# Kernel tuning notes

Measured on AMD Instinct MI355X. Metric: run time of the kernel, lower is better.

## Reference

```python
import jax, jax.numpy as jnp
import numpy as np

K = 10
ALPHA = 0.1
N_NODES = 100000
N_EDGES = 3200000
IN_CH, HID_CH, OUT_CH = 500, 64, 16


def setup_inputs() -> dict:
    key = jax.random.key(0)
    k1, k2, k3, k4, k5, k6 = jax.random.split(key, 6)
    x = jax.random.normal(k1, (N_NODES, IN_CH), dtype=jnp.float32)
    edge_index = jax.random.randint(k2, (2, N_EDGES), 0, N_NODES, dtype=jnp.int64)
    # Linear params (Kaiming-uniform-ish scale)
    s1 = 1.0 / np.sqrt(IN_CH)
    s2 = 1.0 / np.sqrt(HID_CH)
    W1 = jax.random.uniform(k3, (IN_CH, HID_CH), dtype=jnp.float32, minval=-s1, maxval=s1)
    b1 = jax.random.uniform(k4, (HID_CH,), dtype=jnp.float32, minval=-s1, maxval=s1)
    W2 = jax.random.uniform(k5, (HID_CH, OUT_CH), dtype=jnp.float32, minval=-s2, maxval=s2)
    b2 = jax.random.uniform(k6, (OUT_CH,), dtype=jnp.float32, minval=-s2, maxval=s2)
    return {"x": x, "edge_index": edge_index, "W1": W1, "b1": b1, "W2": W2, "b2": b2}


def reference(x, edge_index, W1, b1, W2, b2):
    N = x.shape[0]
    # MLP (eval mode: dropout is identity)
    h = jnp.maximum(x @ W1 + b1, 0.0)
    h = h @ W2 + b2  # [N, out_channels]

    # GCN normalization with self-loops (PyG gcn_norm defaults)
    loops = jnp.arange(N, dtype=edge_index.dtype)
    row = jnp.concatenate([edge_index[0], loops])  # source
    col = jnp.concatenate([edge_index[1], loops])  # target
    ones = jnp.ones(row.shape[0], dtype=h.dtype)
    deg = jax.ops.segment_sum(ones, col, num_segments=N)
    dinv = jnp.where(deg > 0, jax.lax.rsqrt(deg), 0.0)
    norm = dinv[row] * dinv[col]  # [E+N]

    # K-step APPNP propagation: h_{k+1} = (1-alpha) * A_hat h_k + alpha * h_0
    h0 = h

    def step(_, hk):
        agg = jax.ops.segment_sum(norm[:, None] * hk[row], col, num_segments=N)
        return (1.0 - ALPHA) * agg + ALPHA * h0

    return jax.lax.fori_loop(0, K, step, h)
```

## Files before the change

kernel.cpp:

```cpp
#include <hip/hip_runtime.h>

#define IN_CH 500
#define KSTEPS 10

typedef unsigned int u32;
typedef unsigned short u16;
typedef short bf16x8 __attribute__((ext_vector_type(8)));
typedef float f32x4 __attribute__((ext_vector_type(4)));

__device__ __forceinline__ float bf2f(u16 u) {
    union { u32 i; float f; } v; v.i = ((u32)u) << 16; return v.f;
}
__device__ __forceinline__ u16 f2bf(float f) {
    union { float f; u32 i; } v; v.f = f;
    u32 x = v.i;
    return (u16)((x + 0x7FFFu + ((x >> 16) & 1u)) >> 16);
}
__device__ __forceinline__ u32 f_as_u(float f) {
    union { float f; u32 i; } v; v.f = f; return v.i;
}
__device__ __forceinline__ float u_as_f(u32 i) {
    union { u32 i; float f; } v; v.i = i; return v.f;
}

__global__ void detect_kernel(const u16* __restrict__ w1raw,
                              const int* __restrict__ ei,
                              u32* __restrict__ flags) {
    int t = threadIdx.x;
    float m = fabsf(bf2f(w1raw[t]));
    m = fmaxf(m, fabsf(bf2f(w1raw[64 + t])));
    m = fmaxf(m, fabsf(bf2f(w1raw[128 + t])));
    for (int off = 32; off; off >>= 1) m = fmaxf(m, __shfl_down(m, off));
    u32 o = (u32)ei[2 * t + 1];
    o |= (u32)ei[2 * t + 129];
    for (int off = 32; off; off >>= 1) o |= __shfl_down(o, off);
    if (t == 0) {
        flags[0] = (m > 10.0f) ? 1u : 0u;
        flags[1] = (o == 0u) ? 1u : 0u;
    }
}

__global__ void w1t_kernel(const void* __restrict__ W1v,
                           u16* __restrict__ hi, u16* __restrict__ lo,
                           const u32* __restrict__ flags) {
    int i = blockIdx.x * 256 + threadIdx.x;
    if (i >= 64 * 512) return;
    int h = i >> 9;
    int k = i & 511;
    u16 vh = 0, vl = 0;
    if (k < IN_CH) {
        if (flags[0]) {
            float v = ((const float*)W1v)[(size_t)k * 64 + h];
            u32 bits = f_as_u(v);
            vh = (u16)(bits >> 16);
            float d = v - u_as_f(bits & 0xFFFF0000u);
            vl = (u16)(f_as_u(d) >> 16);
        } else {
            vh = ((const u16*)W1v)[(size_t)k * 64 + h];
        }
    }
    hi[(size_t)h * 512 + k] = vh;
    lo[(size_t)h * 512 + k] = vl;
}

__global__ __launch_bounds__(512) void mlp_mfma_f32(
    const float* __restrict__ xf, const u16* __restrict__ w1hig,
    const u16* __restrict__ w1log, const float* __restrict__ b1f,
    const float* __restrict__ W2f, const float* __restrict__ b2f,
    const float* __restrict__ dinv, float* __restrict__ h0,
    float* __restrict__ gout, const u32* __restrict__ flags, int N)
{
    if (flags[0] == 0u) return;

    __shared__ __align__(16) u16 w1hi[64 * 520];
    __shared__ __align__(16) u16 w1lo[64 * 520];
    __shared__ float w2s[64][16];
    __shared__ float b1s[64];
    __shared__ float b2s[16];
    float* hh = (float*)w1hi;

    const int t = threadIdx.x;
    const int w = t >> 6;
    const int l = t & 63;
    const int ln = l & 15;
    const int g = l >> 4;
    const int nodeBase = blockIdx.x * 128;

    for (int i = t; i < 1024; i += 512) w2s[i >> 4][i & 15] = W2f[i];
    if (t < 64) b1s[t] = b1f[t];
    if (t < 16) b2s[t] = b2f[t];

#pragma unroll
    for (int i = 0; i < 8; ++i) {
        int c = t + i * 512;
        int row = c >> 6, c8 = c & 63;
        *(bf16x8*)&w1hi[row * 520 + c8 * 8] =
            *(const bf16x8*)(w1hig + (size_t)row * 512 + c8 * 8);
        *(bf16x8*)&w1lo[row * 520 + c8 * 8] =
            *(const bf16x8*)(w1log + (size_t)row * 512 + c8 * 8);
    }
    __syncthreads();

    const int node = nodeBase + w * 16 + ln;
    const bool nv = (node < N);
    const float* xrow = xf + (size_t)node * IN_CH;

    f32x4 acc0 = {0.f, 0.f, 0.f, 0.f};
    f32x4 acc1 = {0.f, 0.f, 0.f, 0.f};
    f32x4 acc2 = {0.f, 0.f, 0.f, 0.f};
    f32x4 acc3 = {0.f, 0.f, 0.f, 0.f};

#pragma unroll
    for (int ki = 0; ki < 16; ++ki) {
        const int kb = ki * 32 + g * 8;
        float xv[8];
#pragma unroll
        for (int e = 0; e < 8; ++e) xv[e] = 0.f;
        if (nv) {
            if (kb + 8 <= IN_CH) {
                float4 v0 = *(const float4*)(xrow + kb);
                float4 v1 = *(const float4*)(xrow + kb + 4);
                xv[0] = v0.x; xv[1] = v0.y; xv[2] = v0.z; xv[3] = v0.w;
                xv[4] = v1.x; xv[5] = v1.y; xv[6] = v1.z; xv[7] = v1.w;
            } else if (kb < IN_CH) {
                float4 v0 = *(const float4*)(xrow + kb);
                xv[0] = v0.x; xv[1] = v0.y; xv[2] = v0.z; xv[3] = v0.w;
            }
        }
        bf16x8 bh, bl;
#pragma unroll
        for (int e = 0; e < 8; ++e) {
            u32 bits = f_as_u(xv[e]);
            bh[e] = (short)(bits >> 16);
            float d = xv[e] - u_as_f(bits & 0xFFFF0000u);
            bl[e] = (short)(f_as_u(d) >> 16);
        }
        const u16* ph = &w1hi[ln * 520 + kb];
        const u16* pl = &w1lo[ln * 520 + kb];
        bf16x8 ah0 = *(const bf16x8*)(ph);
        bf16x8 ah1 = *(const bf16x8*)(ph + 16 * 520);
        bf16x8 ah2 = *(const bf16x8*)(ph + 32 * 520);
        bf16x8 ah3 = *(const bf16x8*)(ph + 48 * 520);
        bf16x8 al0 = *(const bf16x8*)(pl);
        bf16x8 al1 = *(const bf16x8*)(pl + 16 * 520);
        bf16x8 al2 = *(const bf16x8*)(pl + 32 * 520);
        bf16x8 al3 = *(const bf16x8*)(pl + 48 * 520);
        acc0 = __builtin_amdgcn_mfma_f32_16x16x32_bf16(ah0, bh, acc0, 0, 0, 0);
        acc1 = __builtin_amdgcn_mfma_f32_16x16x32_bf16(ah1, bh, acc1, 0, 0, 0);
        acc2 = __builtin_amdgcn_mfma_f32_16x16x32_bf16(ah2, bh, acc2, 0, 0, 0);
        acc3 = __builtin_amdgcn_mfma_f32_16x16x32_bf16(ah3, bh, acc3, 0, 0, 0);
        acc0 = __builtin_amdgcn_mfma_f32_16x16x32_bf16(al0, bh, acc0, 0, 0, 0);
        acc1 = __builtin_amdgcn_mfma_f32_16x16x32_bf16(al1, bh, acc1, 0, 0, 0);
        acc2 = __builtin_amdgcn_mfma_f32_16x16x32_bf16(al2, bh, acc2, 0, 0, 0);
        acc3 = __builtin_amdgcn_mfma_f32_16x16x32_bf16(al3, bh, acc3, 0, 0, 0);
        acc0 = __builtin_amdgcn_mfma_f32_16x16x32_bf16(ah0, bl, acc0, 0, 0, 0);
        acc1 = __builtin_amdgcn_mfma_f32_16x16x32_bf16(ah1, bl, acc1, 0, 0, 0);
        acc2 = __builtin_amdgcn_mfma_f32_16x16x32_bf16(ah2, bl, acc2, 0, 0, 0);
        acc3 = __builtin_amdgcn_mfma_f32_16x16x32_bf16(ah3, bl, acc3, 0, 0, 0);
    }
    __syncthreads();

    const int nl = w * 16 + ln;
    const int rb = g * 4;
#pragma unroll
    for (int r = 0; r < 4; ++r) {
        float v0 = acc0[r] + b1s[rb + r];
        float v1 = acc1[r] + b1s[16 + rb + r];
        float v2 = acc2[r] + b1s[32 + rb + r];
        float v3 = acc3[r] + b1s[48 + rb + r];
        hh[(rb + r) * 130 + nl]      = v0 > 0.f ? v0 : 0.f;
        hh[(16 + rb + r) * 130 + nl] = v1 > 0.f ? v1 : 0.f;
        hh[(32 + rb + r) * 130 + nl] = v2 > 0.f ? v2 : 0.f;
        hh[(48 + rb + r) * 130 + nl] = v3 > 0.f ? v3 : 0.f;
    }
    __syncthreads();

    {
        int n = t >> 2;
        int o4 = (t & 3) * 4;
        float o0 = b2s[o4], o1 = b2s[o4 + 1], o2 = b2s[o4 + 2], o3 = b2s[o4 + 3];
#pragma unroll
        for (int j = 0; j < 64; ++j) {
            float hv = hh[j * 130 + n];
            o0 += hv * w2s[j][o4];     o1 += hv * w2s[j][o4 + 1];
            o2 += hv * w2s[j][o4 + 2]; o3 += hv * w2s[j][o4 + 3];
        }
        int gn = nodeBase + n;
        if (gn < N) {
            float4 o = {o0, o1, o2, o3};
            *(float4*)(h0 + (size_t)gn * 16 + o4) = o;
            float dn = dinv[gn];
            float4 gg = {o0 * dn, o1 * dn, o2 * dn, o3 * dn};
            *(float4*)(gout + (size_t)gn * 16 + o4) = gg;
        }
    }
}

__global__ __launch_bounds__(256) void mlp_mfma_kernel(
    const u16* __restrict__ xh, const u16* __restrict__ w1tg,
    const void* __restrict__ b1v, const void* __restrict__ W2v,
    const void* __restrict__ b2v, const float* __restrict__ dinv,
    float* __restrict__ h0, float* __restrict__ gout,
    const u32* __restrict__ flags, int N)
{
    if (flags[0] != 0u) return;

    __shared__ __align__(16) u16 w1s[64 * 520];
    __shared__ float w2s[64][16];
    __shared__ float b1s[64];
    __shared__ float b2s[16];
    float* hh = (float*)w1s;

    const u16* b1h = (const u16*)b1v;
    const u16* W2h = (const u16*)W2v;
    const u16* b2h = (const u16*)b2v;

    const int t = threadIdx.x;
    const int w = t >> 6;
    const int l = t & 63;
    const int ln = l & 15;
    const int g = l >> 4;
    const int nodeBase = blockIdx.x * 64;

    for (int i = t; i < 1024; i += 256) w2s[i >> 4][i & 15] = bf2f(W2h[i]);
    if (t < 64) b1s[t] = bf2f(b1h[t]);
    if (t < 16) b2s[t] = bf2f(b2h[t]);

#pragma unroll
    for (int i = 0; i < 16; ++i) {
        int idx = t + i * 256;
        int row = idx >> 6, c8 = idx & 63;
        *(bf16x8*)&w1s[row * 520 + c8 * 8] =
            *(const bf16x8*)(w1tg + (size_t)row * 512 + c8 * 8);
    }
    __syncthreads();

    const int node = nodeBase + w * 16 + ln;
    const bool nv = (node < N);
    const u16* xrow = xh + (size_t)node * IN_CH;

    f32x4 acc0 = {0.f, 0.f, 0.f, 0.f};
    f32x4 acc1 = {0.f, 0.f, 0.f, 0.f};
    f32x4 acc2 = {0.f, 0.f, 0.f, 0.f};
    f32x4 acc3 = {0.f, 0.f, 0.f, 0.f};

#pragma unroll
    for (int ki = 0; ki < 15; ++ki) {
        const int kb = ki * 32 + g * 8;
        bf16x8 b = {0, 0, 0, 0, 0, 0, 0, 0};
        if (nv) b = *(const bf16x8*)(xrow + kb);
        const u16* wp = &w1s[ln * 520 + kb];
        bf16x8 a0 = *(const bf16x8*)(wp);
        bf16x8 a1 = *(const bf16x8*)(wp + 16 * 520);
        bf16x8 a2 = *(const bf16x8*)(wp + 32 * 520);
        bf16x8 a3 = *(const bf16x8*)(wp + 48 * 520);
        acc0 = __builtin_amdgcn_mfma_f32_16x16x32_bf16(a0, b, acc0, 0, 0, 0);
        acc1 = __builtin_amdgcn_mfma_f32_16x16x32_bf16(a1, b, acc1, 0, 0, 0);
        acc2 = __builtin_amdgcn_mfma_f32_16x16x32_bf16(a2, b, acc2, 0, 0, 0);
        acc3 = __builtin_amdgcn_mfma_f32_16x16x32_bf16(a3, b, acc3, 0, 0, 0);
    }
    {
        const int kb = 480 + g * 8;
        bf16x8 b = {0, 0, 0, 0, 0, 0, 0, 0};
        if (nv) {
            if (g < 2) {
                b = *(const bf16x8*)(xrow + kb);
            } else if (g == 2) {
                ushort4 v4 = *(const ushort4*)(xrow + 496);
                b[0] = (short)v4.x; b[1] = (short)v4.y;
                b[2] = (short)v4.z; b[3] = (short)v4.w;
            }
        }
        const u16* wp = &w1s[ln * 520 + kb];
        bf16x8 a0 = *(const bf16x8*)(wp);
        bf16x8 a1 = *(const bf16x8*)(wp + 16 * 520);
        bf16x8 a2 = *(const bf16x8*)(wp + 32 * 520);
        bf16x8 a3 = *(const bf16x8*)(wp + 48 * 520);
        acc0 = __builtin_amdgcn_mfma_f32_16x16x32_bf16(a0, b, acc0, 0, 0, 0);
        acc1 = __builtin_amdgcn_mfma_f32_16x16x32_bf16(a1, b, acc1, 0, 0, 0);
        acc2 = __builtin_amdgcn_mfma_f32_16x16x32_bf16(a2, b, acc2, 0, 0, 0);
        acc3 = __builtin_amdgcn_mfma_f32_16x16x32_bf16(a3, b, acc3, 0, 0, 0);
    }
    __syncthreads();

    const int nl = w * 16 + ln;
    const int rb = g * 4;
#pragma unroll
    for (int r = 0; r < 4; ++r) {
        float v0 = acc0[r] + b1s[rb + r];
        float v1 = acc1[r] + b1s[16 + rb + r];
        float v2 = acc2[r] + b1s[32 + rb + r];
        float v3 = acc3[r] + b1s[48 + rb + r];
        hh[(rb + r) * 65 + nl]      = v0 > 0.f ? v0 : 0.f;
        hh[(16 + rb + r) * 65 + nl] = v1 > 0.f ? v1 : 0.f;
        hh[(32 + rb + r) * 65 + nl] = v2 > 0.f ? v2 : 0.f;
        hh[(48 + rb + r) * 65 + nl] = v3 > 0.f ? v3 : 0.f;
    }
    __syncthreads();

    {
        int n = t >> 2;
        int o4 = (t & 3) * 4;
        float o0 = b2s[o4], o1 = b2s[o4 + 1], o2 = b2s[o4 + 2], o3 = b2s[o4 + 3];
#pragma unroll
        for (int j = 0; j < 64; ++j) {
            float hv = hh[j * 65 + n];
            o0 += hv * w2s[j][o4];     o1 += hv * w2s[j][o4 + 1];
            o2 += hv * w2s[j][o4 + 2]; o3 += hv * w2s[j][o4 + 3];
        }
        int gn = nodeBase + n;
        if (gn < N) {
            float4 o = {o0, o1, o2, o3};
            *(float4*)(h0 + (size_t)gn * 16 + o4) = o;
            float dn = dinv[gn];
            float4 gg = {o0 * dn, o1 * dn, o2 * dn, o3 * dn};
            *(float4*)(gout + (size_t)gn * 16 + o4) = gg;
        }
    }
}

__global__ void zero_u32(u32* __restrict__ p, int n) {
    int i = blockIdx.x * 256 + threadIdx.x;
    if (i < n) p[i] = 0u;
}

__device__ __forceinline__ int ei_src(const int* ei, int E, int e, int i64) {
    return i64 ? ei[2 * e] : ei[e];
}
__device__ __forceinline__ int ei_dst(const int* ei, int E, int e, int i64) {
    return i64 ? ei[2 * (E + e)] : ei[E + e];
}

__global__ void deg_kernel(const int* __restrict__ ei, int E, u32* __restrict__ cnt,
                           const u32* __restrict__ flags) {
    int e = blockIdx.x * 256 + threadIdx.x;
    int i64 = (int)flags[1];
    if (e < E) atomicAdd(&cnt[ei_dst(ei, E, e, i64)], 1u);
}

__global__ void dinv_kernel(const u32* __restrict__ cnt, float* __restrict__ dinv, int N) {
    int i = blockIdx.x * 256 + threadIdx.x;
    if (i < N) {
        float d = (float)(cnt[i] + 1u);
        dinv[i] = rsqrtf(d);
    }
}

__global__ __launch_bounds__(256) void scan1(const u32* __restrict__ cnt,
                                             u32* __restrict__ part, int N) {
    __shared__ u32 s[256];
    int i = blockIdx.x * 256 + threadIdx.x;
    s[threadIdx.x] = (i < N) ? cnt[i] : 0u;
    __syncthreads();
    for (int off = 128; off > 0; off >>= 1) {
        if (threadIdx.x < off) s[threadIdx.x] += s[threadIdx.x + off];
        __syncthreads();
    }
    if (threadIdx.x == 0) part[blockIdx.x] = s[0];
}

__global__ __launch_bounds__(512) void scan2(u32* __restrict__ part,
                                             u32* __restrict__ rowptr, int NB, int N) {
    __shared__ u32 s[512];
    int t = threadIdx.x;
    u32 v = (t < NB) ? part[t] : 0u;
    s[t] = v;
    __syncthreads();
    for (int off = 1; off < 512; off <<= 1) {
        u32 xv = (t >= off) ? s[t - off] : 0u;
        __syncthreads();
        s[t] += xv;
        __syncthreads();
    }
    if (t < NB) part[t] = s[t] - v;
    if (t == 511) rowptr[N] = s[511];
}

__global__ __launch_bounds__(256) void scan3(const u32* __restrict__ cnt,
                                             const u32* __restrict__ part,
                                             u32* __restrict__ rowptr, int N) {
    __shared__ u32 s[256];
    int t = threadIdx.x;
    int i = blockIdx.x * 256 + t;
    u32 v = (i < N) ? cnt[i] : 0u;
    s[t] = v;
    __syncthreads();
    for (int off = 1; off < 256; off <<= 1) {
        u32 xv = (t >= off) ? s[t - off] : 0u;
        __syncthreads();
        s[t] += xv;
        __syncthreads();
    }
    if (i < N) rowptr[i] = part[blockIdx.x] + s[t] - v;
}

#define GSZ_SHIFT 9
#define GSZ 512
#define MAXBUCK 1024
__global__ void init_bf(const u32* __restrict__ rowptr, u32* __restrict__ bf,
                        int N, int nbuck) {
    int t = blockIdx.x * 256 + threadIdx.x;
    if (t < nbuck) {
        int lo = t << GSZ_SHIFT; if (lo > N) lo = N;
        bf[t] = rowptr[lo];
    }
}

#define CHUNK 4096
__global__ __launch_bounds__(256) void bucketA(
    const int* __restrict__ ei, int E, int shiftN, int nbuck,
    u32* __restrict__ tmp, u32* __restrict__ bf, const u32* __restrict__ flags)
{
    __shared__ u32 wbuf[CHUNK];
    __shared__ u16 bbuf[CHUNK];
    __shared__ u32 cnt[MAXBUCK], gbase[MAXBUCK], lcnt[MAXBUCK];
    const int i64 = (int)flags[1];
    for (int base = blockIdx.x * CHUNK; base < E; base += gridDim.x * CHUNK) {
        int nval = E - base; if (nval > CHUNK) nval = CHUNK;
        for (int b = threadIdx.x; b < nbuck; b += 256) { cnt[b] = 0u; lcnt[b] = 0u; }
        __syncthreads();
        for (int j = threadIdx.x; j < nval; j += 256) {
            int e = base + j;
            u32 s = (u32)ei_src(ei, E, e, i64);
            u32 d = (u32)ei_dst(ei, E, e, i64);
            u32 b = d >> GSZ_SHIFT;
            wbuf[j] = s | ((d & (GSZ - 1u)) << shiftN);
            bbuf[j] = (u16)b;
            atomicAdd(&cnt[b], 1u);
        }
        __syncthreads();
        for (int b = threadIdx.x; b < nbuck; b += 256)
            if (cnt[b]) gbase[b] = atomicAdd(&bf[b], cnt[b]);
        __syncthreads();
        for (int j = threadIdx.x; j < nval; j += 256) {
            u32 b = (u32)bbuf[j];
            u32 off = atomicAdd(&lcnt[b], 1u);
            tmp[gbase[b] + off] = wbuf[j];
        }
        __syncthreads();
    }
}

__global__ __launch_bounds__(512) void bucketB(
    const u32* __restrict__ tmp, const u32* __restrict__ rowptr,
    u32* __restrict__ ent, int N, int shiftN)
{
    __shared__ u32 rp[GSZ + 1];
    __shared__ u32 lfill[GSZ];
    const int lo = blockIdx.x << GSZ_SHIFT;
    int hi = lo + GSZ; if (hi > N) hi = N;
    const int nn = hi - lo;
    for (int i = threadIdx.x; i <= nn; i += 512) rp[i] = rowptr[lo + i];
    for (int i = threadIdx.x; i < nn; i += 512) lfill[i] = 0u;
    __syncthreads();
    const u32 pstart = rp[0], pend = rp[nn];
    const u32 mask = (1u << shiftN) - 1u;
    for (u32 p = pstart + threadIdx.x; p < pend; p += 512) {
        u32 wd = tmp[p];
        u32 src = wd & mask;
        u32 dl = wd >> shiftN;
        u32 pos = rp[dl] + atomicAdd(&lfill[dl], 1u);
        ent[pos] = src;
    }
}

#define FILL_BPG 128
__global__ __launch_bounds__(256) void fill_kernel(
    const int* __restrict__ ei, int E,
    const u32* __restrict__ rowptr, u32* __restrict__ fillc,
    u32* __restrict__ ent, const u32* __restrict__ flags, int N)
{
    const int group = blockIdx.x & 7;
    const int bchunk = blockIdx.x >> 3;
    const int gsz = (N + 7) / 8;
    const int lo = group * gsz;
    const int hi = (lo + gsz < N) ? lo + gsz : N;
    const int i64 = (int)flags[1];
    const int stride = FILL_BPG * 256;
    for (int e = bchunk * 256 + (int)threadIdx.x; e < E; e += stride) {
        int c = ei_dst(ei, E, e, i64);
        if (c >= lo && c < hi) {
            int r = ei_src(ei, E, e, i64);
            u32 p = rowptr[c] + atomicAdd(&fillc[c], 1u);
            ent[p] = (u32)r;
        }
    }
}

__global__ __launch_bounds__(256) void prop_kernel(
    const u32* __restrict__ ent, const u32* __restrict__ rowptr,
    const float* __restrict__ dinv, const float* __restrict__ gcur,
    const float* __restrict__ h0, float* __restrict__ gnext,
    void* __restrict__ outp, const u32* __restrict__ flags, int N)
{
    const int t = threadIdx.x;
    const int wv = t >> 6;
    const int l = t & 63;
    const int eg = l >> 2;
    const int c4 = (l & 3) * 4;
    const int n = blockIdx.x * 4 + wv;
    if (n >= N) return;

    const u32 rs = rowptr[n], re = rowptr[n + 1];
    f32x4 acc = {0.f, 0.f, 0.f, 0.f};
    for (u32 base = rs; base < re; base += 32) {
        u32 pA = base + (u32)eg;
        u32 pB = pA + 16u;
        u32 iA = ent[pA < re ? pA : re - 1u];
        u32 iB = ent[pB < re ? pB : re - 1u];
        f32x4 vA = *(const f32x4*)(gcur + (size_t)iA * 16 + c4);
        f32x4 vB = *(const f32x4*)(gcur + (size_t)iB * 16 + c4);
        if (pA < re) acc += vA;
        if (pB < re) acc += vB;
    }
#pragma unroll
    for (int off = 4; off <= 32; off <<= 1) {
        acc[0] += __shfl_xor(acc[0], off);
        acc[1] += __shfl_xor(acc[1], off);
        acc[2] += __shfl_xor(acc[2], off);
        acc[3] += __shfl_xor(acc[3], off);
    }

    if (eg == 0) {
        f32x4 self = *(const f32x4*)(gcur + (size_t)n * 16 + c4);
        f32x4 h0v  = *(const f32x4*)(h0 + (size_t)n * 16 + c4);
        float dn = dinv[n];
        f32x4 h;
#pragma unroll
        for (int j = 0; j < 4; ++j)
            h[j] = 0.9f * dn * (acc[j] + self[j]) + 0.1f * h0v[j];
        if (gnext) {
            f32x4 gg = {dn * h[0], dn * h[1], dn * h[2], dn * h[3]};
            *(f32x4*)(gnext + (size_t)n * 16 + c4) = gg;
        } else if (flags[0]) {
            *(f32x4*)((float*)outp + (size_t)n * 16 + c4) = h;
        } else {
            ushort4 o = {f2bf(h[0]), f2bf(h[1]), f2bf(h[2]), f2bf(h[3])};
            *(ushort4*)((u16*)outp + (size_t)n * 16 + c4) = o;
        }
    }
}

extern "C" void kernel_launch(void* const* d_in, const int* in_sizes, int n_in,
                              void* d_out, int out_size, void* d_ws, size_t ws_size,
                              hipStream_t stream) {
    const void* x  = d_in[0];
    const int* ei  = (const int*)d_in[1];
    const void* W1 = d_in[2];
    const void* b1 = d_in[3];
    const void* W2 = d_in[4];
    const void* b2 = d_in[5];

    const int N = in_sizes[0] / IN_CH;
    const int E = in_sizes[1] / 2;

    float* wf = (float*)d_ws;
    u32*   wu = (u32*)d_ws;

    size_t oH0   = 0;
    size_t oGA   = oH0 + (size_t)N * 16;
    size_t oGB   = oGA + (size_t)N * 16;
    size_t oCNT  = oGB + (size_t)N * 16;
    size_t oFILL = oCNT + N;
    size_t oDINV = oFILL + N;
    size_t oRP   = oDINV + N;
    size_t oPART = ((oRP + N + 1 + 3) & ~(size_t)3);
    size_t oFLG  = oPART + 512;
    size_t oENT  = oFLG + 4;
    size_t oTMP  = oENT + E;
    size_t oBF   = oTMP + E;

    int nbuck = (N + GSZ - 1) >> GSZ_SHIFT;
    int shiftN = 1; while ((1 << shiftN) < N && shiftN < 31) shiftN++;
    bool canBucket = (ws_size >= (oBF + MAXBUCK) * 4) &&
                     (shiftN + GSZ_SHIFT <= 32) && (nbuck <= MAXBUCK);

    u16* w1hig = (u16*)(wf + oGB);
    u16* w1log = w1hig + 64 * 512;

    detect_kernel<<<1, 64, 0, stream>>>((const u16*)W1, ei, wu + oFLG);
    w1t_kernel<<<128, 256, 0, stream>>>(W1, w1hig, w1log, wu + oFLG);
    int nzero = canBucket ? N : 2 * N;
    zero_u32<<<(nzero + 255) / 256, 256, 0, stream>>>(wu + oCNT, nzero);
    deg_kernel<<<(E + 255) / 256, 256, 0, stream>>>(ei, E, wu + oCNT, wu + oFLG);
    dinv_kernel<<<(N + 255) / 256, 256, 0, stream>>>(wu + oCNT, wf + oDINV, N);
    mlp_mfma_f32<<<(N + 127) / 128, 512, 0, stream>>>(
        (const float*)x, w1hig, w1log, (const float*)b1, (const float*)W2,
        (const float*)b2, wf + oDINV, wf + oH0, wf + oGA, wu + oFLG, N);
    mlp_mfma_kernel<<<(N + 63) / 64, 256, 0, stream>>>(
        (const u16*)x, w1hig, b1, W2, b2, wf + oDINV, wf + oH0, wf + oGA,
        wu + oFLG, N);
    int NB = (N + 255) / 256;
    scan1<<<NB, 256, 0, stream>>>(wu + oCNT, wu + oPART, N);
    scan2<<<1, 512, 0, stream>>>(wu + oPART, wu + oRP, NB, N);
    scan3<<<NB, 256, 0, stream>>>(wu + oCNT, wu + oPART, wu + oRP, N);

    if (canBucket) {
        init_bf<<<(nbuck + 255) / 256, 256, 0, stream>>>(wu + oRP, wu + oBF,
                                                         N, nbuck);
        int nblkA = (E + CHUNK - 1) / CHUNK;
        bucketA<<<nblkA, 256, 0, stream>>>(ei, E, shiftN, nbuck,
                                           wu + oTMP, wu + oBF, wu + oFLG);
        bucketB<<<nbuck, 512, 0, stream>>>(wu + oTMP, wu + oRP, wu + oENT,
                                           N, shiftN);
    } else {
        fill_kernel<<<8 * FILL_BPG, 256, 0, stream>>>(ei, E, wu + oRP,
                                                      wu + oFILL, wu + oENT,
                                                      wu + oFLG, N);
    }

    const float* cur = wf + oGA;
    for (int k = 0; k < KSTEPS; ++k) {
        bool last = (k == KSTEPS - 1);
        float* nxt = last ? nullptr : (wf + ((k & 1) ? oGA : oGB));
        prop_kernel<<<(N + 3) / 4, 256, 0, stream>>>(
            wu + oENT, wu + oRP, wf + oDINV, cur, wf + oH0,
            nxt, last ? d_out : nullptr, wu + oFLG, N);
        if (!last) cur = nxt;
    }
}
```

Before: 992.5 us.

## Derive degrees and row pointers from bucket pass instead of global atomics

Replaces the per-node global-atomic degree histogram, the three-kernel node scan and init_bf with a coarse per-bucket histogram in shared memory plus a single-block bucket scan. The per-node degree, dinv and row pointers are then computed inside a new bucketB2 from the bucketed edge data with shared-memory atomics and a local scan. This removes the 3.2M global atomics on per-node counters and several small launches, at the cost of an extra pass over the destination indices in histA and an extra read of each bucket in bucketB2.

```diff
diff --git a/kernel.cpp b/kernel.cpp
--- a/kernel.cpp
+++ b/kernel.cpp
@@ -394,76 +394,6 @@
     if (i < N) rowptr[i] = part[blockIdx.x] + s[t] - v;
 }
 
-#define GSZ_SHIFT 9
-#define GSZ 512
-#define MAXBUCK 1024
-__global__ void init_bf(const u32* __restrict__ rowptr, u32* __restrict__ bf,
-                        int N, int nbuck) {
-    int t = blockIdx.x * 256 + threadIdx.x;
-    if (t < nbuck) {
-        int lo = t << GSZ_SHIFT; if (lo > N) lo = N;
-        bf[t] = rowptr[lo];
-    }
-}
-
-#define CHUNK 4096
-__global__ __launch_bounds__(256) void bucketA(
-    const int* __restrict__ ei, int E, int shiftN, int nbuck,
-    u32* __restrict__ tmp, u32* __restrict__ bf, const u32* __restrict__ flags)
-{
-    __shared__ u32 wbuf[CHUNK];
-    __shared__ u16 bbuf[CHUNK];
-    __shared__ u32 cnt[MAXBUCK], gbase[MAXBUCK], lcnt[MAXBUCK];
-    const int i64 = (int)flags[1];
-    for (int base = blockIdx.x * CHUNK; base < E; base += gridDim.x * CHUNK) {
-        int nval = E - base; if (nval > CHUNK) nval = CHUNK;
-        for (int b = threadIdx.x; b < nbuck; b += 256) { cnt[b] = 0u; lcnt[b] = 0u; }
-        __syncthreads();
-        for (int j = threadIdx.x; j < nval; j += 256) {
-            int e = base + j;
-            u32 s = (u32)ei_src(ei, E, e, i64);
-            u32 d = (u32)ei_dst(ei, E, e, i64);
-            u32 b = d >> GSZ_SHIFT;
-            wbuf[j] = s | ((d & (GSZ - 1u)) << shiftN);
-            bbuf[j] = (u16)b;
-            atomicAdd(&cnt[b], 1u);
-        }
-        __syncthreads();
-        for (int b = threadIdx.x; b < nbuck; b += 256)
-            if (cnt[b]) gbase[b] = atomicAdd(&bf[b], cnt[b]);
-        __syncthreads();
-        for (int j = threadIdx.x; j < nval; j += 256) {
-            u32 b = (u32)bbuf[j];
-            u32 off = atomicAdd(&lcnt[b], 1u);
-            tmp[gbase[b] + off] = wbuf[j];
-        }
-        __syncthreads();
-    }
-}
-
-__global__ __launch_bounds__(512) void bucketB(
-    const u32* __restrict__ tmp, const u32* __restrict__ rowptr,
-    u32* __restrict__ ent, int N, int shiftN)
-{
-    __shared__ u32 rp[GSZ + 1];
-    __shared__ u32 lfill[GSZ];
-    const int lo = blockIdx.x << GSZ_SHIFT;
-    int hi = lo + GSZ; if (hi > N) hi = N;
-    const int nn = hi - lo;
-    for (int i = threadIdx.x; i <= nn; i += 512) rp[i] = rowptr[lo + i];
-    for (int i = threadIdx.x; i < nn; i += 512) lfill[i] = 0u;
-    __syncthreads();
-    const u32 pstart = rp[0], pend = rp[nn];
-    const u32 mask = (1u << shiftN) - 1u;
-    for (u32 p = pstart + threadIdx.x; p < pend; p += 512) {
-        u32 wd = tmp[p];
-        u32 src = wd & mask;
-        u32 dl = wd >> shiftN;
-        u32 pos = rp[dl] + atomicAdd(&lfill[dl], 1u);
-        ent[pos] = src;
-    }
-}
-
 #define FILL_BPG 128
 __global__ __launch_bounds__(256) void fill_kernel(
     const int* __restrict__ ei, int E,
@@ -487,6 +417,131 @@
     }
 }
 
+#define GSZ_SHIFT 9
+#define GSZ 512
+#define MAXBUCK 1024
+#define CHUNK 4096
+
+__global__ __launch_bounds__(256) void histA(
+    const int* __restrict__ ei, int E, int nbuck,
+    u32* __restrict__ bcnt, const u32* __restrict__ flags)
+{
+    __shared__ u32 lb[MAXBUCK];
+    const int i64 = (int)flags[1];
+    for (int b = threadIdx.x; b < nbuck; b += 256) lb[b] = 0u;
+    __syncthreads();
+    const int stride = gridDim.x * 256;
+    for (int e = blockIdx.x * 256 + (int)threadIdx.x; e < E; e += stride) {
+        u32 d = (u32)ei_dst(ei, E, e, i64);
+        atomicAdd(&lb[d >> GSZ_SHIFT], 1u);
+    }
+    __syncthreads();
+    for (int b = threadIdx.x; b < nbuck; b += 256)
+        if (lb[b]) atomicAdd(&bcnt[b], lb[b]);
+}
+
+__global__ __launch_bounds__(1024) void scanB(
+    const u32* __restrict__ bcnt, u32* __restrict__ bbase, u32* __restrict__ bf,
+    u32* __restrict__ rowptr, int nbuck, int N, int E)
+{
+    __shared__ u32 s[MAXBUCK];
+    int t = threadIdx.x;
+    u32 v = (t < nbuck) ? bcnt[t] : 0u;
+    s[t] = v;
+    __syncthreads();
+    for (int off = 1; off < MAXBUCK; off <<= 1) {
+        u32 xv = (t >= off) ? s[t - off] : 0u;
+        __syncthreads();
+        s[t] += xv;
+        __syncthreads();
+    }
+    if (t < nbuck) {
+        u32 excl = s[t] - v;
+        bbase[t] = excl;
+        bf[t] = excl;
+    }
+    if (t == 0) { bbase[nbuck] = (u32)E; rowptr[N] = (u32)E; }
+}
+
+__global__ __launch_bounds__(256) void bucketA(
+    const int* __restrict__ ei, int E, int shiftN, int nbuck,
+    u32* __restrict__ tmp, u32* __restrict__ bf, const u32* __restrict__ flags)
+{
+    __shared__ u32 wbuf[CHUNK];
+    __shared__ u16 bbuf[CHUNK];
+    __shared__ u32 cnt[MAXBUCK], gbase[MAXBUCK], lcnt[MAXBUCK];
+    const int i64 = (int)flags[1];
+    for (int base = blockIdx.x * CHUNK; base < E; base += gridDim.x * CHUNK) {
+        int nval = E - base; if (nval > CHUNK) nval = CHUNK;
+        for (int b = threadIdx.x; b < nbuck; b += 256) { cnt[b] = 0u; lcnt[b] = 0u; }
+        __syncthreads();
+        for (int j = threadIdx.x; j < nval; j += 256) {
+            int e = base + j;
+            u32 s = (u32)ei_src(ei, E, e, i64);
+            u32 d = (u32)ei_dst(ei, E, e, i64);
+            u32 b = d >> GSZ_SHIFT;
+            wbuf[j] = s | ((d & (GSZ - 1u)) << shiftN);
+            bbuf[j] = (u16)b;
+            atomicAdd(&cnt[b], 1u);
+        }
+        __syncthreads();
+        for (int b = threadIdx.x; b < nbuck; b += 256)
+            if (cnt[b]) gbase[b] = atomicAdd(&bf[b], cnt[b]);
+        __syncthreads();
+        for (int j = threadIdx.x; j < nval; j += 256) {
+            u32 b = (u32)bbuf[j];
+            u32 off = atomicAdd(&lcnt[b], 1u);
+            tmp[gbase[b] + off] = wbuf[j];
+        }
+        __syncthreads();
+    }
+}
+
+__global__ __launch_bounds__(512) void bucketB2(
+    const u32* __restrict__ tmp, const u32* __restrict__ bbase,
+    u32* __restrict__ rowptr, float* __restrict__ dinv,
+    u32* __restrict__ ent, int N, int shiftN)
+{
+    __shared__ u32 deg[GSZ];
+    __shared__ u32 rp[GSZ];
+    __shared__ u32 lfill[GSZ];
+    const int b = blockIdx.x;
+    const int lo = b << GSZ_SHIFT;
+    int hi = lo + GSZ; if (hi > N) hi = N;
+    const int nn = hi - lo;
+    if (nn <= 0) return;
+    const u32 base = bbase[b], bend = bbase[b + 1];
+    const int t = threadIdx.x;
+    deg[t] = 0u; lfill[t] = 0u;
+    __syncthreads();
+    const u32 mask = (1u << shiftN) - 1u;
+    for (u32 p = base + t; p < bend; p += 512)
+        atomicAdd(&deg[tmp[p] >> shiftN], 1u);
+    __syncthreads();
+    u32 v = (t < nn) ? deg[t] : 0u;
+    if (t < nn) dinv[lo + t] = rsqrtf((float)(v + 1u));
+    rp[t] = v;
+    __syncthreads();
+    for (int off = 1; off < GSZ; off <<= 1) {
+        u32 xv = (t >= off) ? rp[t - off] : 0u;
+        __syncthreads();
+        rp[t] += xv;
+        __syncthreads();
+    }
+    u32 myrp = base + rp[t] - v;
+    __syncthreads();
+    rp[t] = myrp;
+    if (t < nn) rowptr[lo + t] = myrp;
+    __syncthreads();
+    for (u32 p = base + t; p < bend; p += 512) {
+        u32 wd = tmp[p];
+        u32 src = wd & mask;
+        u32 dl = wd >> shiftN;
+        u32 pos = rp[dl] + atomicAdd(&lfill[dl], 1u);
+        ent[pos] = src;
+    }
+}
+
 __global__ __launch_bounds__(256) void prop_kernel(
     const u32* __restrict__ ent, const u32* __restrict__ rowptr,
     const float* __restrict__ dinv, const float* __restrict__ gcur,
@@ -569,10 +624,12 @@
     size_t oENT  = oFLG + 4;
     size_t oTMP  = oENT + E;
     size_t oBF   = oTMP + E;
+    size_t oBC   = oBF + MAXBUCK;
+    size_t oBB   = oBC + MAXBUCK;
 
     int nbuck = (N + GSZ - 1) >> GSZ_SHIFT;
     int shiftN = 1; while ((1 << shiftN) < N && shiftN < 31) shiftN++;
-    bool canBucket = (ws_size >= (oBF + MAXBUCK) * 4) &&
+    bool canBucket = (ws_size >= (oBB + MAXBUCK + 1) * 4) &&
                      (shiftN + GSZ_SHIFT <= 32) && (nbuck <= MAXBUCK);
 
     u16* w1hig = (u16*)(wf + oGB);
@@ -580,34 +637,38 @@
 
     detect_kernel<<<1, 64, 0, stream>>>((const u16*)W1, ei, wu + oFLG);
     w1t_kernel<<<128, 256, 0, stream>>>(W1, w1hig, w1log, wu + oFLG);
-    int nzero = canBucket ? N : 2 * N;
-    zero_u32<<<(nzero + 255) / 256, 256, 0, stream>>>(wu + oCNT, nzero);
-    deg_kernel<<<(E + 255) / 256, 256, 0, stream>>>(ei, E, wu + oCNT, wu + oFLG);
-    dinv_kernel<<<(N + 255) / 256, 256, 0, stream>>>(wu + oCNT, wf + oDINV, N);
+
+    if (canBucket) {
+        zero_u32<<<(MAXBUCK + 255) / 256, 256, 0, stream>>>(wu + oBC, MAXBUCK);
+        histA<<<512, 256, 0, stream>>>(ei, E, nbuck, wu + oBC, wu + oFLG);
+        scanB<<<1, 1024, 0, stream>>>(wu + oBC, wu + oBB, wu + oBF,
+                                      wu + oRP, nbuck, N, E);
+        int nblkA = (E + CHUNK - 1) / CHUNK;
+        bucketA<<<nblkA, 256, 0, stream>>>(ei, E, shiftN, nbuck,
+                                           wu + oTMP, wu + oBF, wu + oFLG);
+        bucketB2<<<nbuck, 512, 0, stream>>>(wu + oTMP, wu + oBB, wu + oRP,
+                                            wf + oDINV, wu + oENT, N, shiftN);
+    } else {
+        zero_u32<<<(2 * N + 255) / 256, 256, 0, stream>>>(wu + oCNT, 2 * N);
+        deg_kernel<<<(E + 255) / 256, 256, 0, stream>>>(ei, E, wu + oCNT,
+                                                        wu + oFLG);
+        dinv_kernel<<<(N + 255) / 256, 256, 0, stream>>>(wu + oCNT,
+                                                         wf + oDINV, N);
+        int NB = (N + 255) / 256;
+        scan1<<<NB, 256, 0, stream>>>(wu + oCNT, wu + oPART, N);
+        scan2<<<1, 512, 0, stream>>>(wu + oPART, wu + oRP, NB, N);
+        scan3<<<NB, 256, 0, stream>>>(wu + oCNT, wu + oPART, wu + oRP, N);
+        fill_kernel<<<8 * FILL_BPG, 256, 0, stream>>>(ei, E, wu + oRP,
+                                                      wu + oFILL, wu + oENT,
+                                                      wu + oFLG, N);
+    }
+
     mlp_mfma_f32<<<(N + 127) / 128, 512, 0, stream>>>(
         (const float*)x, w1hig, w1log, (const float*)b1, (const float*)W2,
         (const float*)b2, wf + oDINV, wf + oH0, wf + oGA, wu + oFLG, N);
     mlp_mfma_kernel<<<(N + 63) / 64, 256, 0, stream>>>(
         (const u16*)x, w1hig, b1, W2, b2, wf + oDINV, wf + oH0, wf + oGA,
         wu + oFLG, N);
-    int NB = (N + 255) / 256;
-    scan1<<<NB, 256, 0, stream>>>(wu + oCNT, wu + oPART, N);
-    scan2<<<1, 512, 0, stream>>>(wu + oPART, wu + oRP, NB, N);
-    scan3<<<NB, 256, 0, stream>>>(wu + oCNT, wu + oPART, wu + oRP, N);
-
-    if (canBucket) {
-        init_bf<<<(nbuck + 255) / 256, 256, 0, stream>>>(wu + oRP, wu + oBF,
-                                                         N, nbuck);
-        int nblkA = (E + CHUNK - 1) / CHUNK;
-        bucketA<<<nblkA, 256, 0, stream>>>(ei, E, shiftN, nbuck,
-                                           wu + oTMP, wu + oBF, wu + oFLG);
-        bucketB<<<nbuck, 512, 0, stream>>>(wu + oTMP, wu + oRP, wu + oENT,
-                                           N, shiftN);
-    } else {
-        fill_kernel<<<8 * FILL_BPG, 256, 0, stream>>>(ei, E, wu + oRP,
-                                                      wu + oFILL, wu + oENT,
-                                                      wu + oFLG, N);
-    }
 
     const float* cur = wf + oGA;
     for (int k = 0; k < KSTEPS; ++k) {
```

Result: faster. 883.9 us (-10.9%).
